# Performance work log

Hardware: AMD Instinct MI355X
Metric: run time of the kernel (lower is better)

The kernel has to match this reference:

```python
import jax, jax.numpy as jnp
import numpy as np
from jax import lax

B, N, C = 8, 8192, 64
ODR, K, OUT = 4, 32, 128
S = N // ODR
EPS = 1e-5


def _lbr(h, W, b, g, be):
    # h: [M, K, Cin] -> linear -> BN (training-mode batch stats over (M,K) per channel) -> relu
    y = jnp.einsum('mki,oi->mko', h, W) + b
    mean = y.mean(axis=(0, 1))
    var = ((y - mean) ** 2).mean(axis=(0, 1))  # biased var, as torch BN uses for normalization
    y = (y - mean) * lax.rsqrt(var + EPS) * g + be
    return jax.nn.relu(y)


def setup_inputs() -> dict:
    key = jax.random.key(0)
    ks = jax.random.split(key, 12)
    x = jax.random.normal(ks[0], (B, N, C), dtype=jnp.float32)
    coor = jax.random.normal(ks[1], (B, N, 3), dtype=jnp.float32)
    indx = jax.random.permutation(ks[2], N)[:S]  # like torch.randperm(N)[:S]
    w1 = jax.random.normal(ks[3], (OUT, 2 * C), dtype=jnp.float32) * (2 * C) ** -0.5
    b1 = jax.random.normal(ks[4], (OUT,), dtype=jnp.float32) * 0.01
    g1 = jax.random.uniform(ks[5], (OUT,), dtype=jnp.float32, minval=0.5, maxval=1.5)
    be1 = jax.random.normal(ks[6], (OUT,), dtype=jnp.float32) * 0.01
    w2 = jax.random.normal(ks[7], (OUT, OUT), dtype=jnp.float32) * OUT ** -0.5
    b2 = jax.random.normal(ks[8], (OUT,), dtype=jnp.float32) * 0.01
    g2 = jax.random.uniform(ks[9], (OUT,), dtype=jnp.float32, minval=0.5, maxval=1.5)
    be2 = jax.random.normal(ks[10], (OUT,), dtype=jnp.float32) * 0.01
    return dict(x=x, coor=coor, indx=indx, w1=w1, b1=b1, g1=g1, be1=be1,
                w2=w2, b2=b2, g2=g2, be2=be2)


def reference(x, coor, indx, w1, b1, g1, be1, w2, b2, g2, be2):
    sampled_coor = coor[:, indx, :]  # [B,S,3]
    sampled_x = x[:, indx, :]        # [B,S,C]
    # pairwise squared distances [B,S,N]
    dist = jnp.sum((coor[:, None, :, :] - sampled_coor[:, :, None, :]) ** 2, axis=-1)
    # k smallest distances == argsort(dist)[..., :K]
    _, knn_idx = lax.top_k(-dist, K)  # [B,S,K]
    knn_x = jax.vmap(lambda xb, ib: xb[ib])(x, knn_idx)  # [B,S,K,C]
    rep_x = jnp.broadcast_to(sampled_x[:, :, None, :], (x.shape[0], S, K, x.shape[2]))
    feat = jnp.concatenate([rep_x, knn_x - rep_x], axis=-1)  # [B,S,K,2C]
    feat = feat.reshape(x.shape[0] * S, K, 2 * x.shape[2])
    h = _lbr(feat, w1, b1, g1, be1)
    h = _lbr(h, w2, b2, g2, be2)
    h = h.reshape(x.shape[0], S, K, -1)
    out = jnp.max(h, axis=2)  # [B,S,OUT]
    return out, sampled_coor
```

## Files before the change

### kernel.cpp

```cpp
#include <hip/hip_runtime.h>
#include <stdint.h>


#define N_    8192
#define GPB_  8

typedef __attribute__((ext_vector_type(8))) short bf8;
typedef __attribute__((ext_vector_type(16))) float f32x16;
typedef __attribute__((ext_vector_type(2))) float f32x2;

__device__ __forceinline__ unsigned int bf1u(float f) {
  unsigned int u = __float_as_uint(f);
  return (u + 0x7fffu + ((u >> 16) & 1u)) >> 16;
}
__device__ __forceinline__ unsigned int bfpair(float lo, float hi) {
  return bf1u(lo) | (bf1u(hi) << 16);
}

__device__ __forceinline__ f32x2 pk_add(f32x2 a, f32x2 b) {
  f32x2 d;
  asm("v_pk_add_f32 %0, %1, %2" : "=v"(d) : "v"(a), "v"(b));
  return d;
}
__device__ __forceinline__ f32x2 pk_mul(f32x2 a, f32x2 b) {
  f32x2 d;
  asm("v_pk_mul_f32 %0, %1, %2" : "=v"(d) : "v"(a), "v"(b));
  return d;
}

__global__ __launch_bounds__(256) void kprep(const float* __restrict__ w1,
                                             const float* __restrict__ w2,
                                             const float* __restrict__ coor,
                                             const int* __restrict__ indx,
                                             unsigned short* __restrict__ w1b,
                                             unsigned short* __restrict__ w2b,
                                             float* __restrict__ outc,
                                             float* __restrict__ soa) {
  int e = blockIdx.x * 256 + threadIdx.x;
  if (e < 16384) {
    w1b[e] = (unsigned short)bf1u(w1[e]);
  } else if (e < 32768) {
    int e2 = e - 16384;
    w2b[e2] = (unsigned short)bf1u(w2[e2]);
  } else if (e < 81920) {
    int e2 = e - 32768;
    int bs = e2 / 3, c = e2 - bs * 3;
    int b = bs >> 11, s = bs & 2047;
    outc[e2] = coor[(b * N_ + indx[s]) * 3 + c];
  } else {
    int p = e - 81920;
    const int b = p >> 13, i = p & 8191;
    const float* src = coor + (size_t)p * 3;
    float* dst = soa + b * 24576;
    dst[i]         = src[0];
    dst[8192 + i]  = src[1];
    dst[16384 + i] = src[2];
  }
}

__global__ __launch_bounds__(256, 8) void kknn(const float* __restrict__ soa,
                                               const int* __restrict__ indx,
                                               int* __restrict__ knn) {
  __shared__ __align__(16) float4 sdist4[4 * 256];
  __shared__ float sTw[4];
  __shared__ unsigned long long cands[192];
  __shared__ int ccnt;

  const int gid = blockIdx.x;
  const int b = gid >> 11, s = gid & 2047;
  const int tid = threadIdx.x;
  const int w = tid >> 6, lane = tid & 63;
  const float* Xb = soa + b * 24576;
  const float* Yb = Xb + 8192;
  const float* Zb = Xb + 16384;
  const int qi = indx[s];
  const float qx = Xb[qi], qy = Yb[qi], qz = Zb[qi];
  const f32x2 nqx = {-qx, -qx}, nqy = {-qy, -qy}, nqz = {-qz, -qz};

  f32x2 rd[8];
  float dmA = 3.4e38f, dmB = 3.4e38f;
#pragma unroll
  for (int it = 0; it < 8; ++it) {
    const int ofs = (it << 10) + (tid << 2);
    union { float4 f4; f32x2 h[2]; } X, Y, Z;
    X.f4 = *(const float4*)(Xb + ofs);
    Y.f4 = *(const float4*)(Yb + ofs);
    Z.f4 = *(const float4*)(Zb + ofs);
    const f32x2 dxl = pk_add(X.h[0], nqx), dyl = pk_add(Y.h[0], nqy),
                dzl = pk_add(Z.h[0], nqz);
    const f32x2 dxh = pk_add(X.h[1], nqx), dyh = pk_add(Y.h[1], nqy),
                dzh = pk_add(Z.h[1], nqz);
    const f32x2 sl =
        pk_add(pk_add(pk_mul(dxl, dxl), pk_mul(dyl, dyl)), pk_mul(dzl, dzl));
    const f32x2 sh =
        pk_add(pk_add(pk_mul(dxh, dxh), pk_mul(dyh, dyh)), pk_mul(dzh, dzh));
    dmA = fminf(fminf(sl.x, sl.y), dmA);
    dmB = fminf(fminf(sh.x, sh.y), dmB);
    if (it < 4) {
      rd[it * 2] = sl;
      rd[it * 2 + 1] = sh;
    } else {
      union { float4 f4; f32x2 h[2]; } st;
      st.h[0] = sl;
      st.h[1] = sh;
      sdist4[((it - 4) << 8) + tid] = st.f4;
    }
  }
  float dmin = fminf(dmA, dmB);
  if (tid == 0) ccnt = 0;
  if (tid < 192) cands[tid] = ~0ULL;

  float v = dmin;
#pragma unroll
  for (int k = 2; k <= 64; k <<= 1) {
#pragma unroll
    for (int j = k >> 1; j >= 1; j >>= 1) {
      const float o = __shfl_xor(v, j, 64);
      const bool dirAsc = ((lane & k) == 0);
      const bool lower = ((lane & j) == 0);
      const float lo = fminf(v, o), hi = fmaxf(v, o);
      v = (dirAsc == lower) ? lo : hi;
    }
  }
  if (lane == 7) sTw[w] = v;
  __syncthreads();
  const float T = fmaxf(fmaxf(sTw[0], sTw[1]), fmaxf(sTw[2], sTw[3]));

#pragma unroll
  for (int t = 0; t < 8; ++t) {
    const int p0 = ((t >> 1) << 10) + (tid << 2) + ((t & 1) << 1);
    const float d0 = rd[t].x, d1 = rd[t].y;
    if (d0 <= T) {
      const int pos = atomicAdd(&ccnt, 1);
      if (pos < 192)
        cands[pos] = ((unsigned long long)__float_as_uint(d0) << 32) |
                     (unsigned int)p0;
    }
    if (d1 <= T) {
      const int pos = atomicAdd(&ccnt, 1);
      if (pos < 192)
        cands[pos] = ((unsigned long long)__float_as_uint(d1) << 32) |
                     (unsigned int)(p0 + 1);
    }
  }
#pragma unroll
  for (int it = 4; it < 8; ++it) {
    const float4 d4 = sdist4[((it - 4) << 8) + tid];
    const int p0 = (it << 10) + (tid << 2);
    const float dd[4] = {d4.x, d4.y, d4.z, d4.w};
#pragma unroll
    for (int j = 0; j < 4; ++j) {
      if (dd[j] <= T) {
        const int pos = atomicAdd(&ccnt, 1);
        if (pos < 192)
          cands[pos] = ((unsigned long long)__float_as_uint(dd[j]) << 32) |
                       (unsigned int)(p0 + j);
      }
    }
  }
  __syncthreads();

  const int E = min(ccnt, 192);
  if (tid < E) {
    const unsigned long long key = cands[tid];
    int rank = 0;
    for (int j = 0; j < E; ++j) rank += (cands[j] < key) ? 1 : 0;
    if (rank < 32) knn[gid * 32 + rank] = (int)(unsigned int)key;
  }
}

template <int PHASE>
__global__ __launch_bounds__(256, 2) void kphase(
    const float* __restrict__ x, const int* __restrict__ indx,
    const int* __restrict__ knn, const float* __restrict__ b1,
    const unsigned short* __restrict__ w1b, const unsigned short* __restrict__ w2b,
    const float* __restrict__ b2, const float* __restrict__ st1,
    float* __restrict__ part, float* __restrict__ mout) {
  __shared__ __align__(16) unsigned short sxb[2][80];
  __shared__ __align__(16) unsigned short dls[2][32 * 68 + 8];
  __shared__ __align__(16) unsigned short h1[PHASE == 2 ? 2 * 32 * 136 : 8];

  const int tid = threadIdx.x;
  const int w = tid >> 6;
  const int lane = tid & 63;
  const int m = lane & 31, q2 = lane >> 5;
  const int col = (w << 5) + m;
  const int r8 = tid >> 3, c8 = (tid & 7) * 8;

  const int bb = blockIdx.x & 7;
  const int jj = blockIdx.x >> 3;
  const float* xb = x + (size_t)bb * (N_ * 64);
  const int gidbase = (bb << 11) + jj * GPB_;
  const int sbase = jj * GPB_;

  bf8 bf1[8];
#pragma unroll
  for (int t = 0; t < 8; ++t)
    bf1[t] = *(const bf8*)&w1b[col * 128 + t * 16 + q2 * 8];
  bf8 bf2[8];
  float s1 = 0.f, t1 = 0.f, b2v = 0.f;
  if constexpr (PHASE == 2) {
#pragma unroll
    for (int t = 0; t < 8; ++t)
      bf2[t] = *(const bf8*)&w2b[col * 128 + t * 16 + q2 * 8];
    s1 = st1[col];
    t1 = st1[128 + col];
    b2v = b2[col];
  }
  (void)w2b; (void)b2; (void)st1; (void)mout;
  const float b1c = b1[col];

  float sum = 0.f, ssq = 0.f;

  float4 ca_c, cc_c, ga_c, gc_c;
  {
    const int idx0 = indx[sbase];
    const int nbr0 = knn[(size_t)gidbase * 32 + r8];
    const float* c0 = xb + (size_t)idx0 * 64;
    ca_c = *(const float4*)(c0 + c8);
    cc_c = *(const float4*)(c0 + c8 + 4);
    const float* g0 = xb + (size_t)nbr0 * 64;
    ga_c = *(const float4*)(g0 + c8);
    gc_c = *(const float4*)(g0 + c8 + 4);
  }
  int idx_nxt = (GPB_ > 1) ? indx[sbase + 1] : 0;
  int nbr_nxt = (GPB_ > 1) ? knn[(size_t)(gidbase + 1) * 32 + r8] : 0;

#pragma unroll 1
  for (int g = 0; g < GPB_; ++g) {
    const int gid = gidbase + g;
    const int p = g & 1;

    float4 ca_n = ca_c, cc_n = cc_c, ga_n = ga_c, gc_n = gc_c;
    if (g + 1 < GPB_) {
      const float* cn = xb + (size_t)idx_nxt * 64;
      ca_n = *(const float4*)(cn + c8);
      cc_n = *(const float4*)(cn + c8 + 4);
      const float* gn = xb + (size_t)nbr_nxt * 64;
      ga_n = *(const float4*)(gn + c8);
      gc_n = *(const float4*)(gn + c8 + 4);
    }
    if (g + 2 < GPB_) {
      nbr_nxt = knn[(size_t)(gid + 2) * 32 + r8];
      idx_nxt = indx[sbase + g + 2];
    }

    {
      uint2 lo, hi;
      lo.x = bfpair(ga_c.x - ca_c.x, ga_c.y - ca_c.y);
      lo.y = bfpair(ga_c.z - ca_c.z, ga_c.w - ca_c.w);
      hi.x = bfpair(gc_c.x - cc_c.x, gc_c.y - cc_c.y);
      hi.y = bfpair(gc_c.z - cc_c.z, gc_c.w - cc_c.w);
      *(uint2*)&dls[p][r8 * 68 + c8] = lo;
      *(uint2*)&dls[p][r8 * 68 + c8 + 4] = hi;
    }
    if (tid < 8) {
      uint2 lo, hi;
      lo.x = bfpair(ca_c.x, ca_c.y);
      lo.y = bfpair(ca_c.z, ca_c.w);
      hi.x = bfpair(cc_c.x, cc_c.y);
      hi.y = bfpair(cc_c.z, cc_c.w);
      *(uint2*)&sxb[p][tid * 8] = lo;
      *(uint2*)&sxb[p][tid * 8 + 4] = hi;
    }
    asm volatile("s_waitcnt lgkmcnt(0)" ::: "memory");
    __builtin_amdgcn_s_barrier();

    bf8 af[8];
#pragma unroll
    for (int t = 0; t < 4; ++t) {
      union { bf8 v; uint2 u[2]; } fa;
      fa.u[0] = *(const uint2*)&sxb[p][t * 16 + q2 * 8];
      fa.u[1] = *(const uint2*)&sxb[p][t * 16 + q2 * 8 + 4];
      af[t] = fa.v;
    }
#pragma unroll
    for (int t = 0; t < 4; ++t) {
      union { bf8 v; uint2 u[2]; } fa;
      fa.u[0] = *(const uint2*)&dls[p][m * 68 + t * 16 + q2 * 8];
      fa.u[1] = *(const uint2*)&dls[p][m * 68 + t * 16 + q2 * 8 + 4];
      af[4 + t] = fa.v;
    }

    f32x16 acc;
#pragma unroll
    for (int r = 0; r < 16; ++r) acc[r] = b1c;
#pragma unroll
    for (int t = 0; t < 8; ++t)
      acc = __builtin_amdgcn_mfma_f32_32x32x16_bf16(af[t], bf1[t], acc, 0, 0, 0);

    if constexpr (PHASE == 1) {
#pragma unroll
      for (int r = 0; r < 16; ++r) {
        const float v = acc[r];
        sum += v;
        ssq = fmaf(v, v, ssq);
      }
    } else {
      const int hp = p * (32 * 136);
#pragma unroll
      for (int r = 0; r < 16; ++r) {
        const float hv = fmaxf(0.f, fmaf(acc[r], s1, t1));
        const int row = (r & 3) + ((r >> 2) << 3) + (q2 << 2);
        h1[hp + row * 136 + col] = (unsigned short)bf1u(hv);
      }
      asm volatile("s_waitcnt lgkmcnt(0)" ::: "memory");
      __builtin_amdgcn_s_barrier();

      f32x16 acc2;
#pragma unroll
      for (int r = 0; r < 16; ++r) acc2[r] = b2v;
#pragma unroll
      for (int t = 0; t < 8; ++t) {
        const bf8 a2 = *(const bf8*)&h1[hp + m * 136 + t * 16 + q2 * 8];
        acc2 = __builtin_amdgcn_mfma_f32_32x32x16_bf16(a2, bf2[t], acc2, 0, 0, 0);
      }

      float mx = -1e30f;
#pragma unroll
      for (int r = 0; r < 16; ++r) {
        const float v = acc2[r];
        sum += v;
        ssq = fmaf(v, v, ssq);
        mx = fmaxf(mx, v);
      }
      mx = fmaxf(mx, __shfl_xor(mx, 32, 64));
      if (lane < 32) mout[(size_t)gid * 128 + col] = mx;
    }

    ca_c = ca_n;
    cc_c = cc_n;
    ga_c = ga_n;
    gc_c = gc_n;
  }

  sum += __shfl_xor(sum, 32, 64);
  ssq += __shfl_xor(ssq, 32, 64);
  if (lane < 32) {
    part[blockIdx.x * 256 + col] = sum;
    part[blockIdx.x * 256 + 128 + col] = ssq;
  }
}

__global__ __launch_bounds__(256) void kred1(const float* __restrict__ part,
                                             double* __restrict__ dbuf) {
  const int blk = blockIdx.x;
  const int c = threadIdx.x;
  const float* p = part + (size_t)blk * 32 * 256 + c;
  double acc = 0.0;
#pragma unroll 8
  for (int r = 0; r < 32; ++r) acc += (double)p[r * 256];
  dbuf[blk * 256 + c] = acc;
}

__global__ __launch_bounds__(256) void kred2(const double* __restrict__ dbuf,
                                             const float* __restrict__ gam,
                                             const float* __restrict__ bet,
                                             float* __restrict__ st) {
  __shared__ double sS[256];
  const int c = threadIdx.x;
  double acc = 0.0;
#pragma unroll 8
  for (int i = 0; i < 64; ++i) acc += dbuf[i * 256 + c];
  sS[c] = acc;
  __syncthreads();
  if (c < 128) {
    const double Sv = sS[c], SSv = sS[128 + c];
    const double cnt = 524288.0;
    const double mean = Sv / cnt;
    const double var = SSv / cnt - mean * mean;
    const double scale = (double)gam[c] / sqrt(var + 1e-5);
    st[c] = (float)scale;
    st[128 + c] = (float)((double)bet[c] - mean * scale);
  }
}

__global__ __launch_bounds__(256) void kout(const float* __restrict__ m,
                                            const float* __restrict__ st2,
                                            float* __restrict__ out) {
  const int e4 = blockIdx.x * 256 + threadIdx.x;
  const int o0 = (e4 & 31) * 4;
  const float4 v = ((const float4*)m)[e4];
  const float4 sc = *(const float4*)&st2[o0];
  const float4 sh = *(const float4*)&st2[128 + o0];
  float4 r;
  r.x = fmaxf(0.f, fmaf(v.x, sc.x, sh.x));
  r.y = fmaxf(0.f, fmaf(v.y, sc.y, sh.y));
  r.z = fmaxf(0.f, fmaf(v.z, sc.z, sh.z));
  r.w = fmaxf(0.f, fmaf(v.w, sc.w, sh.w));
  ((float4*)out)[e4] = r;
}

extern "C" void kernel_launch(void* const* d_in, const int* in_sizes, int n_in,
                              void* d_out, int out_size, void* d_ws, size_t ws_size,
                              hipStream_t stream) {
  (void)in_sizes; (void)n_in; (void)out_size; (void)ws_size;
  const float* x    = (const float*)d_in[0];
  const float* coor = (const float*)d_in[1];
  const int*   indx = (const int*)d_in[2];
  const float* w1   = (const float*)d_in[3];
  const float* b1   = (const float*)d_in[4];
  const float* g1   = (const float*)d_in[5];
  const float* be1  = (const float*)d_in[6];
  const float* w2   = (const float*)d_in[7];
  const float* b2   = (const float*)d_in[8];
  const float* g2   = (const float*)d_in[9];
  const float* be2  = (const float*)d_in[10];
  float* out = (float*)d_out;

  char* ws = (char*)d_ws;
  int*            knn   = (int*)(ws + 0);
  float*          mbuf  = (float*)(ws + 2097152);
  float*          part1 = (float*)(ws + 10485760);
  float*          soa   = (float*)(ws + 10485760);
  float*          part2 = (float*)(ws + 12582912);
  unsigned short* w1b   = (unsigned short*)(ws + 14680064);
  unsigned short* w2b   = (unsigned short*)(ws + 14712832);
  float*          st1   = (float*)(ws + 14745600);
  float*          st2   = (float*)(ws + 14746624);
  double*         dbuf  = (double*)(ws + 14747648);

  float* outc = out + 2097152;

  kprep<<<576, 256, 0, stream>>>(w1, w2, coor, indx, w1b, w2b, outc, soa);
  kknn<<<16384, 256, 0, stream>>>(soa, indx, knn);
  kphase<1><<<2048, 256, 0, stream>>>(x, indx, knn, b1, w1b, w2b, b2, nullptr,
                                      part1, nullptr);
  kred1<<<64, 256, 0, stream>>>(part1, dbuf);
  kred2<<<1, 256, 0, stream>>>(dbuf, g1, be1, st1);
  kphase<2><<<2048, 256, 0, stream>>>(x, indx, knn, b1, w1b, w2b, b2, st1,
                                      part2, mbuf);
  kred1<<<64, 256, 0, stream>>>(part2, dbuf);
  kred2<<<1, 256, 0, stream>>>(dbuf, g2, be2, st2);
  kout<<<2048, 256, 0, stream>>>(mbuf, st2, out);
}
```

Baseline: 245.6 us.

## Replace shared atomic candidate compaction with per-wave ballot; double groups per phase block

The kNN kernel used a shared-memory atomicAdd counter for every candidate below the threshold. It now compacts candidates within each wave using ballot and mbcnt into a private 48-slot segment per wave, and ranks over all 192 slots while skipping empty ones. This removes the LDS atomic contention but caps each wave at 48 candidates, so a single wave holding many of the true neighbours could drop some. Separately, the phase kernels process 16 groups per block with half as many blocks, and the partial-sum reduction is adjusted to match.

```diff
diff --git a/kernel.cpp b/kernel.cpp
--- a/kernel.cpp
+++ b/kernel.cpp
@@ -3,7 +3,7 @@
 
 
 #define N_    8192
-#define GPB_  8
+#define GPB_  16
 
 typedef __attribute__((ext_vector_type(8))) short bf8;
 typedef __attribute__((ext_vector_type(16))) float f32x16;
@@ -64,7 +64,6 @@
   __shared__ __align__(16) float4 sdist4[4 * 256];
   __shared__ float sTw[4];
   __shared__ unsigned long long cands[192];
-  __shared__ int ccnt;
 
   const int gid = blockIdx.x;
   const int b = gid >> 11, s = gid & 2047;
@@ -107,7 +106,6 @@
     }
   }
   float dmin = fminf(dmA, dmB);
-  if (tid == 0) ccnt = 0;
   if (tid < 192) cands[tid] = ~0ULL;
 
   float v = dmin;
@@ -126,21 +124,27 @@
   __syncthreads();
   const float T = fmaxf(fmaxf(sTw[0], sTw[1]), fmaxf(sTw[2], sTw[3]));
 
+  int wbase = 0;
+  const int cbase = w * 48;
 #pragma unroll
   for (int t = 0; t < 8; ++t) {
     const int p0 = ((t >> 1) << 10) + (tid << 2) + ((t & 1) << 1);
-    const float d0 = rd[t].x, d1 = rd[t].y;
-    if (d0 <= T) {
-      const int pos = atomicAdd(&ccnt, 1);
-      if (pos < 192)
-        cands[pos] = ((unsigned long long)__float_as_uint(d0) << 32) |
-                     (unsigned int)p0;
-    }
-    if (d1 <= T) {
-      const int pos = atomicAdd(&ccnt, 1);
-      if (pos < 192)
-        cands[pos] = ((unsigned long long)__float_as_uint(d1) << 32) |
-                     (unsigned int)(p0 + 1);
+#pragma unroll
+    for (int c2 = 0; c2 < 2; ++c2) {
+      const float d = (c2 == 0) ? rd[t].x : rd[t].y;
+      const bool pr = (d <= T);
+      const unsigned long long mk = __ballot(pr);
+      if (pr) {
+        const int mb = __builtin_amdgcn_mbcnt_hi(
+            (unsigned int)(mk >> 32),
+            __builtin_amdgcn_mbcnt_lo((unsigned int)mk, 0));
+        const int pos = wbase + mb;
+        if (pos < 48)
+          cands[cbase + pos] =
+              ((unsigned long long)__float_as_uint(d) << 32) |
+              (unsigned int)(p0 + c2);
+      }
+      wbase += (int)__popcll(mk);
     }
   }
 #pragma unroll
@@ -150,22 +154,32 @@
     const float dd[4] = {d4.x, d4.y, d4.z, d4.w};
 #pragma unroll
     for (int j = 0; j < 4; ++j) {
-      if (dd[j] <= T) {
-        const int pos = atomicAdd(&ccnt, 1);
-        if (pos < 192)
-          cands[pos] = ((unsigned long long)__float_as_uint(dd[j]) << 32) |
-                       (unsigned int)(p0 + j);
-      }
+      const float d = dd[j];
+      const bool pr = (d <= T);
+      const unsigned long long mk = __ballot(pr);
+      if (pr) {
+        const int mb = __builtin_amdgcn_mbcnt_hi(
+            (unsigned int)(mk >> 32),
+            __builtin_amdgcn_mbcnt_lo((unsigned int)mk, 0));
+        const int pos = wbase + mb;
+        if (pos < 48)
+          cands[cbase + pos] =
+              ((unsigned long long)__float_as_uint(d) << 32) |
+              (unsigned int)(p0 + j);
+      }
+      wbase += (int)__popcll(mk);
     }
   }
   __syncthreads();
 
-  const int E = min(ccnt, 192);
-  if (tid < E) {
+  if (tid < 192) {
     const unsigned long long key = cands[tid];
-    int rank = 0;
-    for (int j = 0; j < E; ++j) rank += (cands[j] < key) ? 1 : 0;
-    if (rank < 32) knn[gid * 32 + rank] = (int)(unsigned int)key;
+    if (key != ~0ULL) {
+      int rank = 0;
+#pragma unroll 8
+      for (int j = 0; j < 192; ++j) rank += (cands[j] < key) ? 1 : 0;
+      if (rank < 32) knn[gid * 32 + rank] = (int)(unsigned int)key;
+    }
   }
 }
 
@@ -346,10 +360,10 @@
                                              double* __restrict__ dbuf) {
   const int blk = blockIdx.x;
   const int c = threadIdx.x;
-  const float* p = part + (size_t)blk * 32 * 256 + c;
+  const float* p = part + (size_t)blk * 16 * 256 + c;
   double acc = 0.0;
-#pragma unroll 8
-  for (int r = 0; r < 32; ++r) acc += (double)p[r * 256];
+#pragma unroll
+  for (int r = 0; r < 16; ++r) acc += (double)p[r * 256];
   dbuf[blk * 256 + c] = acc;
 }
 
@@ -424,11 +438,11 @@
 
   kprep<<<576, 256, 0, stream>>>(w1, w2, coor, indx, w1b, w2b, outc, soa);
   kknn<<<16384, 256, 0, stream>>>(soa, indx, knn);
-  kphase<1><<<2048, 256, 0, stream>>>(x, indx, knn, b1, w1b, w2b, b2, nullptr,
+  kphase<1><<<1024, 256, 0, stream>>>(x, indx, knn, b1, w1b, w2b, b2, nullptr,
                                       part1, nullptr);
   kred1<<<64, 256, 0, stream>>>(part1, dbuf);
   kred2<<<1, 256, 0, stream>>>(dbuf, g1, be1, st1);
-  kphase<2><<<2048, 256, 0, stream>>>(x, indx, knn, b1, w1b, w2b, b2, st1,
+  kphase<2><<<1024, 256, 0, stream>>>(x, indx, knn, b1, w1b, w2b, b2, st1,
                                       part2, mbuf);
   kred1<<<64, 256, 0, stream>>>(part2, dbuf);
   kred2<<<1, 256, 0, stream>>>(dbuf, g2, be2, st2);
```

Result: slower. 263.0 us (+7.1%).
